# Kernel tuning notes

Measured on AMD Instinct MI355X. Metric: run time of the kernel, lower is better.

The kernel has to match this reference:

```python
import math
import jax, jax.numpy as jnp
import numpy as np

EPS = 1e-12

def _layernorm(x, g, b):
    u = x.mean(-1, keepdims=True)
    s = ((x - u) ** 2).mean(-1, keepdims=True)
    return g * (x - u) / jnp.sqrt(s + EPS) + b

def _sinusoidal_pe(S, d):
    pos = np.arange(S, dtype=np.float32)[:, None]
    div = np.exp(np.arange(0, d, 2, dtype=np.float32) * -(math.log(10000.0) / d))
    pe = np.zeros((S, d), dtype=np.float32)
    pe[:, 0::2] = np.sin(pos * div)
    pe[:, 1::2] = np.cos(pos * div)
    return jnp.asarray(pe)

def setup_inputs() -> dict:
    key = jax.random.key(0)
    k1, k2, k3, k4 = jax.random.split(key, 4)
    B, L, V, Dw, H = 32, 2048, 30522, 300, 768
    P = 16                      # separator period -> S = L // P ingredients per row
    S = L // P
    ids = jax.random.randint(k1, (B, L), 1, V).astype(jnp.int32)
    sep = np.zeros((B, L), dtype=np.int32)
    sep[:, P - 1::P] = 1        # a separator token every P tokens
    emb_table = jax.random.normal(k2, (V, Dw), dtype=jnp.float32) * 0.02
    emb_table = emb_table.at[0].set(0.0)  # padding_idx=0
    W = jax.random.normal(k3, (Dw, H), dtype=jnp.float32) * 0.02
    b = jnp.zeros((H,), dtype=jnp.float32)
    return {
        "ingr_input_ids": ids,
        "ingr_sep_masks": jnp.asarray(sep),
        "num_ingr": S,
        "emb_table": emb_table,
        "ln1_g": jnp.ones((Dw,), jnp.float32),
        "ln1_b": jnp.zeros((Dw,), jnp.float32),
        "W": W,
        "b": b,
        "ln2_g": jnp.ones((H,), jnp.float32),
        "ln2_b": jnp.zeros((H,), jnp.float32),
    }

def reference(ingr_input_ids, ingr_sep_masks, num_ingr,
              emb_table, ln1_g, ln1_b, W, b, ln2_g, ln2_b):
    S = int(num_ingr)
    H = W.shape[1]
    # embed + LN + Linear + ReLU + LN (dropout is identity at eval)
    e = emb_table[ingr_input_ids]                       # [B, L, Dw]
    h = _layernorm(e, ln1_g, ln1_b)
    h = jax.nn.relu(jnp.einsum('bld,dh->blh', h, W) + b)
    h = _layernorm(h, ln2_g, ln2_b)                     # [B, L, H]
    # ragged segment mean: segment id = exclusive cumsum of sep mask;
    # separator tokens (out[:-1] in the original) are excluded from the mean;
    # tokens after the last separator fall into bucket S and are dropped.
    sep = ingr_sep_masks
    seg = jnp.cumsum(sep, axis=1) - sep                 # [B, L]
    seg = jnp.minimum(seg, S)
    valid = (1 - sep).astype(h.dtype)                   # [B, L]
    seg_sum = jax.vmap(lambda hh, ss: jax.ops.segment_sum(hh, ss, num_segments=S + 1))(
        h * valid[..., None], seg)                      # [B, S+1, H]
    seg_cnt = jax.vmap(lambda vv, ss: jax.ops.segment_sum(vv, ss, num_segments=S + 1))(
        valid, seg)                                     # [B, S+1]
    mean = jnp.where(seg_cnt[..., None] > 0,
                     seg_sum / jnp.maximum(seg_cnt, 1.0)[..., None],
                     0.0)[:, :S]                        # [B, S, H]
    return mean + _sinusoidal_pe(S, H)[None]
```

## Files before the change

kernel.cpp:

```cpp
#include <hip/hip_runtime.h>
#include <hip/hip_bf16.h>

#define B_   32
#define L_   2048
#define V_   30522
#define DW   300
#define H_   768
#define KP   320
#define NT   (H_/16)
#define KT   (KP/32)
#define VPAD 30528
#define MB   48
#define NW   6
#define APAD 336

typedef __attribute__((ext_vector_type(8))) short bf16x8;
typedef __attribute__((ext_vector_type(4))) float f32x4;

__global__ void pack_w(const float* __restrict__ W, __hip_bfloat16* __restrict__ Wp) {
    int t = blockIdx.x * 256 + threadIdx.x;
    if (t >= NT * KT * 64) return;
    int lane = t & 63;
    int f    = t >> 6;
    int n    = f % NT;
    int kt   = f / NT;
    int col  = n * 16 + (lane & 15);
    int k0   = kt * 32 + (lane >> 4) * 8;
    union { __hip_bfloat16 h[8]; int4 v; } u;
    #pragma unroll
    for (int j = 0; j < 8; ++j) {
        int k = k0 + j;
        float w = (k < DW) ? W[(size_t)k * H_ + col] : 0.f;
        u.h[j] = __float2bfloat16(w);
    }
    reinterpret_cast<int4*>(Wp)[t] = u.v;
}

__global__ void embed_ln1(const float* __restrict__ emb, const float* __restrict__ g1,
                          const float* __restrict__ b1, __hip_bfloat16* __restrict__ h1) {
    int wave = (blockIdx.x * blockDim.x + threadIdx.x) >> 6;
    int lane = threadIdx.x & 63;
    if (wave >= VPAD) return;
    __hip_bfloat16* dst = h1 + (size_t)wave * KP;
    if (wave >= V_) {
        for (int k = lane; k < KP; k += 64) dst[k] = __float2bfloat16(0.f);
        return;
    }
    const float* row = emb + (size_t)wave * DW;
    float x[5]; float s = 0.f, ss = 0.f;
    #pragma unroll
    for (int i = 0; i < 5; ++i) {
        int k = lane + i * 64;
        float v = (k < DW) ? row[k] : 0.f;
        x[i] = v; s += v; ss += v * v;
    }
    #pragma unroll
    for (int m = 32; m >= 1; m >>= 1) { s += __shfl_xor(s, m); ss += __shfl_xor(ss, m); }
    float mu   = s / (float)DW;
    float var  = ss / (float)DW - mu * mu;
    float rstd = rsqrtf(var + 1e-12f);
    #pragma unroll
    for (int i = 0; i < 5; ++i) {
        int k = lane + i * 64;
        float o = (k < DW) ? (g1[k] * ((x[i] - mu) * rstd) + b1[k]) : 0.f;
        dst[k] = __float2bfloat16(o);
    }
}

__global__ void __launch_bounds__(512, 2)
gemm_ln2(const __hip_bfloat16* __restrict__ h1, const __hip_bfloat16* __restrict__ Wp,
         const float* __restrict__ bias, const float* __restrict__ g2,
         const float* __restrict__ b2, __hip_bfloat16* __restrict__ G) {
    __shared__ __hip_bfloat16 sA[MB * APAD];
    __shared__ float sred[2][8][MB];
    int tid  = threadIdx.x;
    int w    = tid >> 6;
    int lane = tid & 63;
    int r = lane & 15, q = lane >> 4;
    size_t row0 = (size_t)blockIdx.x * MB;

    const int4* gsrc = reinterpret_cast<const int4*>(h1 + row0 * KP);
    #pragma unroll
    for (int i = 0; i < 4; ++i) {
        int t4 = tid + i * 512;
        if (t4 < MB * KP / 8) {
            int row = t4 / 40;
            int col = (t4 % 40) * 8;
            *reinterpret_cast<int4*>(&sA[row * APAD + col]) = gsrc[t4];
        }
    }

    f32x4 acc[NW][3];
    #pragma unroll
    for (int nl = 0; nl < NW; ++nl)
        #pragma unroll
        for (int m = 0; m < 3; ++m) acc[nl][m] = (f32x4){0.f, 0.f, 0.f, 0.f};

    const bf16x8* Bv = reinterpret_cast<const bf16x8*>(Wp) + (size_t)w * NW * 64 + lane;
    const char* sAc = reinterpret_cast<const char*>(sA);
    const int abase = r * (APAD * 2) + q * 16;
    int phase = (int)(blockIdx.x % KT);

    bf16x8 bbuf[2][NW];
    bf16x8 abuf[2][3];

    {
        const bf16x8* bp = Bv + (size_t)phase * NT * 64;
        #pragma unroll
        for (int nl = 0; nl < NW; ++nl) bbuf[0][nl] = bp[nl * 64];
    }
    __syncthreads();
    #pragma unroll
    for (int m = 0; m < 3; ++m)
        abuf[0][m] = *reinterpret_cast<const bf16x8*>(
            sAc + abase + m * (16 * APAD * 2) + phase * 64);

    #pragma unroll
    for (int i = 0; i < KT; ++i) {
        const int cur = i & 1, nxt = (i + 1) & 1;
        if (i + 1 < KT) {
            int ktn = phase + i + 1; if (ktn >= KT) ktn -= KT;
            const bf16x8* bp = Bv + (size_t)ktn * NT * 64;
            #pragma unroll
            for (int nl = 0; nl < NW; ++nl) bbuf[nxt][nl] = bp[nl * 64];
            #pragma unroll
            for (int m = 0; m < 3; ++m)
                abuf[nxt][m] = *reinterpret_cast<const bf16x8*>(
                    sAc + abase + m * (16 * APAD * 2) + ktn * 64);
        }
        __builtin_amdgcn_sched_barrier(0);
        #pragma unroll
        for (int nl = 0; nl < NW; ++nl) {
            acc[nl][0] = __builtin_amdgcn_mfma_f32_16x16x32_bf16(abuf[cur][0], bbuf[cur][nl], acc[nl][0], 0, 0, 0);
            acc[nl][1] = __builtin_amdgcn_mfma_f32_16x16x32_bf16(abuf[cur][1], bbuf[cur][nl], acc[nl][1], 0, 0, 0);
            acc[nl][2] = __builtin_amdgcn_mfma_f32_16x16x32_bf16(abuf[cur][2], bbuf[cur][nl], acc[nl][2], 0, 0, 0);
        }
    }

    float s_[3][4], ss_[3][4];
    #pragma unroll
    for (int m = 0; m < 3; ++m)
        #pragma unroll
        for (int j = 0; j < 4; ++j) { s_[m][j] = 0.f; ss_[m][j] = 0.f; }
    #pragma unroll
    for (int nl = 0; nl < NW; ++nl) {
        float bn = bias[w * 96 + nl * 16 + r];
        #pragma unroll
        for (int m = 0; m < 3; ++m)
            #pragma unroll
            for (int j = 0; j < 4; ++j) {
                float v = acc[nl][m][j] + bn;
                v = v > 0.f ? v : 0.f;
                acc[nl][m][j] = v;
                s_[m][j] += v; ss_[m][j] += v * v;
            }
    }
    #pragma unroll
    for (int msk = 1; msk < 16; msk <<= 1)
        #pragma unroll
        for (int m = 0; m < 3; ++m)
            #pragma unroll
            for (int j = 0; j < 4; ++j) {
                s_[m][j]  += __shfl_xor(s_[m][j],  msk);
                ss_[m][j] += __shfl_xor(ss_[m][j], msk);
            }
    if (r == 0) {
        #pragma unroll
        for (int m = 0; m < 3; ++m)
            #pragma unroll
            for (int j = 0; j < 4; ++j) {
                int row = m * 16 + q * 4 + j;
                sred[0][w][row] = s_[m][j];
                sred[1][w][row] = ss_[m][j];
            }
    }
    __syncthreads();

    #pragma unroll
    for (int m = 0; m < 3; ++m) {
        #pragma unroll
        for (int j = 0; j < 4; ++j) {
            int row = m * 16 + q * 4 + j;
            float ts = 0.f, tss = 0.f;
            #pragma unroll
            for (int ww = 0; ww < 8; ++ww) { ts += sred[0][ww][row]; tss += sred[1][ww][row]; }
            float mu   = ts / (float)H_;
            float var  = tss / (float)H_ - mu * mu;
            float rstd = rsqrtf(var + 1e-12f);
            s_[m][j]  = mu;
            ss_[m][j] = rstd;
        }
    }
    #pragma unroll
    for (int nl = 0; nl < NW; ++nl) {
        int col = w * 96 + nl * 16 + r;
        float gg = g2[col], bb = b2[col];
        #pragma unroll
        for (int m = 0; m < 3; ++m)
            #pragma unroll
            for (int j = 0; j < 4; ++j) {
                size_t rowg = row0 + m * 16 + q * 4 + j;
                float val = gg * (acc[nl][m][j] - s_[m][j]) * ss_[m][j] + bb;
                G[rowg * H_ + col] = __float2bfloat16(val);
            }
    }
}

__global__ void sep_scan(const int* __restrict__ sep, int* __restrict__ pos, int* __restrict__ nsep) {
    int b = blockIdx.x;
    const int* row = sep + (size_t)b * L_;
    __shared__ int cnt[256];
    int tid = threadIdx.x;
    int local[8]; int c = 0;
    #pragma unroll
    for (int i = 0; i < 8; ++i) { int v = row[tid * 8 + i]; local[i] = v; c += v; }
    cnt[tid] = c; __syncthreads();
    for (int ofs = 1; ofs < 256; ofs <<= 1) {
        int v = (tid >= ofs) ? cnt[tid - ofs] : 0;
        __syncthreads();
        cnt[tid] += v;
        __syncthreads();
    }
    int w = cnt[tid] - c;
    #pragma unroll
    for (int i = 0; i < 8; ++i)
        if (local[i]) { pos[(size_t)b * L_ + w] = tid * 8 + i; ++w; }
    if (tid == 255) nsep[b] = cnt[255];
}

__global__ void seg_gather(const int* __restrict__ ids, const int* __restrict__ pos,
                           const int* __restrict__ nsep, const __hip_bfloat16* __restrict__ G,
                           float* __restrict__ out, int S) {
    int blk = blockIdx.x;
    int s = blk % S, b = blk / S;
    int tid = threadIdx.x;
    int ns = nsep[b];
    int lo, hi;
    if (s > ns) { lo = 1; hi = 0; }
    else {
        lo = (s == 0) ? 0 : pos[(size_t)b * L_ + (s - 1)] + 1;
        hi = (s < ns) ? pos[(size_t)b * L_ + s] - 1 : L_ - 1;
    }
    int cnt = hi - lo + 1; if (cnt < 0) cnt = 0;
    float a0 = 0.f, a1 = 0.f, a2 = 0.f;
    for (int t = lo; t <= hi; ++t) {
        int v = ids[(size_t)b * L_ + t];
        const __hip_bfloat16* gr = G + (size_t)v * H_;
        a0 += __bfloat162float(gr[tid]);
        a1 += __bfloat162float(gr[tid + 256]);
        a2 += __bfloat162float(gr[tid + 512]);
    }
    float inv = (cnt > 0) ? 1.f / (float)cnt : 0.f;
    float* orow = out + ((size_t)b * S + s) * H_;
    const float cexp = -9.210340371976184f / (float)H_;
    float acc[3] = {a0, a1, a2};
    #pragma unroll
    for (int c = 0; c < 3; ++c) {
        int n = tid + c * 256;
        int i = n >> 1;
        float div = expf((float)(2 * i) * cexp);
        float ang = (float)s * div;
        float pe  = (n & 1) ? cosf(ang) : sinf(ang);
        orow[n] = acc[c] * inv + pe;
    }
}

extern "C" void kernel_launch(void* const* d_in, const int* in_sizes, int n_in,
                              void* d_out, int out_size, void* d_ws, size_t ws_size,
                              hipStream_t stream) {
    const int*   ids  = (const int*)d_in[0];
    const int*   sep  = (const int*)d_in[1];
    const float* emb  = (const float*)d_in[3];
    const float* g1   = (const float*)d_in[4];
    const float* b1   = (const float*)d_in[5];
    const float* W    = (const float*)d_in[6];
    const float* bias = (const float*)d_in[7];
    const float* g2   = (const float*)d_in[8];
    const float* b2   = (const float*)d_in[9];
    float* out = (float*)d_out;

    int S = out_size / (B_ * H_);

    char* ws = (char*)d_ws;
    __hip_bfloat16* Wp  = (__hip_bfloat16*)(ws);
    __hip_bfloat16* h1  = (__hip_bfloat16*)(ws + 491520);
    __hip_bfloat16* G   = (__hip_bfloat16*)(ws + 491520 + 19537920);
    int* pos  = (int*)(ws + 491520 + 19537920 + 46891008);
    int* nsep = (int*)(ws + 491520 + 19537920 + 46891008 + 262144);
    (void)ws_size; (void)n_in; (void)in_sizes;

    pack_w   <<<(NT * KT * 64 + 255) / 256, 256, 0, stream>>>(W, Wp);
    embed_ln1<<<VPAD / 4, 256, 0, stream>>>(emb, g1, b1, h1);
    gemm_ln2 <<<VPAD / MB, 512, 0, stream>>>(h1, Wp, bias, g2, b2, G);
    sep_scan <<<B_, 256, 0, stream>>>(sep, pos, nsep);
    seg_gather<<<B_ * S, 256, 0, stream>>>(ids, pos, nsep, G, out, S);
}
```

Baseline: 82.92 us.

## Deepen GEMM B prefetch, vectorize segment gather, precompute PE table

The GEMM inner loop now keeps a 4-deep register ring for the W fragments, prefetching three K-steps ahead instead of one, so global-load latency is better hidden behind the MFMAs. seg_gather is restructured so 192 threads each read 16-byte vectors of the bf16 row, split the tokens between two groups and reduce through shared memory, replacing scalar 2-byte loads. Sinusoidal positional encodings are computed once by a new small kernel into workspace, so seg_gather no longer evaluates expf/sinf/cosf per element. The costs are extra register pressure in the GEMM, 64 idle threads per gather block, and one more kernel launch.

```diff
diff --git a/kernel.cpp b/kernel.cpp
--- a/kernel.cpp
+++ b/kernel.cpp
@@ -101,15 +101,17 @@
     const int abase = r * (APAD * 2) + q * 16;
     int phase = (int)(blockIdx.x % KT);
 
-    bf16x8 bbuf[2][NW];
+    bf16x8 bbuf[4][NW];
     bf16x8 abuf[2][3];
 
-    {
-        const bf16x8* bp = Bv + (size_t)phase * NT * 64;
-        #pragma unroll
-        for (int nl = 0; nl < NW; ++nl) bbuf[0][nl] = bp[nl * 64];
-    }
     __syncthreads();
+    #pragma unroll
+    for (int p = 0; p < 3; ++p) {
+        int ktp = phase + p; if (ktp >= KT) ktp -= KT;
+        const bf16x8* bp = Bv + (size_t)ktp * NT * 64;
+        #pragma unroll
+        for (int nl = 0; nl < NW; ++nl) bbuf[p][nl] = bp[nl * 64];
+    }
     #pragma unroll
     for (int m = 0; m < 3; ++m)
         abuf[0][m] = *reinterpret_cast<const bf16x8*>(
@@ -117,23 +119,26 @@
 
     #pragma unroll
     for (int i = 0; i < KT; ++i) {
-        const int cur = i & 1, nxt = (i + 1) & 1;
+        const int cur = i & 3, acur = i & 1;
+        if (i + 3 < KT) {
+            int ktn = phase + i + 3; if (ktn >= KT) ktn -= KT;
+            const bf16x8* bp = Bv + (size_t)ktn * NT * 64;
+            #pragma unroll
+            for (int nl = 0; nl < NW; ++nl) bbuf[(i + 3) & 3][nl] = bp[nl * 64];
+        }
         if (i + 1 < KT) {
             int ktn = phase + i + 1; if (ktn >= KT) ktn -= KT;
-            const bf16x8* bp = Bv + (size_t)ktn * NT * 64;
-            #pragma unroll
-            for (int nl = 0; nl < NW; ++nl) bbuf[nxt][nl] = bp[nl * 64];
             #pragma unroll
             for (int m = 0; m < 3; ++m)
-                abuf[nxt][m] = *reinterpret_cast<const bf16x8*>(
+                abuf[(i + 1) & 1][m] = *reinterpret_cast<const bf16x8*>(
                     sAc + abase + m * (16 * APAD * 2) + ktn * 64);
         }
         __builtin_amdgcn_sched_barrier(0);
         #pragma unroll
         for (int nl = 0; nl < NW; ++nl) {
-            acc[nl][0] = __builtin_amdgcn_mfma_f32_16x16x32_bf16(abuf[cur][0], bbuf[cur][nl], acc[nl][0], 0, 0, 0);
-            acc[nl][1] = __builtin_amdgcn_mfma_f32_16x16x32_bf16(abuf[cur][1], bbuf[cur][nl], acc[nl][1], 0, 0, 0);
-            acc[nl][2] = __builtin_amdgcn_mfma_f32_16x16x32_bf16(abuf[cur][2], bbuf[cur][nl], acc[nl][2], 0, 0, 0);
+            acc[nl][0] = __builtin_amdgcn_mfma_f32_16x16x32_bf16(abuf[acur][0], bbuf[cur][nl], acc[nl][0], 0, 0, 0);
+            acc[nl][1] = __builtin_amdgcn_mfma_f32_16x16x32_bf16(abuf[acur][1], bbuf[cur][nl], acc[nl][1], 0, 0, 0);
+            acc[nl][2] = __builtin_amdgcn_mfma_f32_16x16x32_bf16(abuf[acur][2], bbuf[cur][nl], acc[nl][2], 0, 0, 0);
         }
     }
 
@@ -228,12 +233,23 @@
     if (tid == 255) nsep[b] = cnt[255];
 }
 
+__global__ void pe_table(float* __restrict__ PE, int S) {
+    int t = blockIdx.x * 256 + threadIdx.x;
+    if (t >= S * H_) return;
+    int s = t / H_, n = t % H_;
+    const float cexp = -9.210340371976184f / (float)H_;
+    float div = expf((float)(2 * (n >> 1)) * cexp);
+    float ang = (float)s * div;
+    PE[t] = (n & 1) ? cosf(ang) : sinf(ang);
+}
+
 __global__ void seg_gather(const int* __restrict__ ids, const int* __restrict__ pos,
                            const int* __restrict__ nsep, const __hip_bfloat16* __restrict__ G,
-                           float* __restrict__ out, int S) {
+                           const float* __restrict__ PE, float* __restrict__ out, int S) {
     int blk = blockIdx.x;
     int s = blk % S, b = blk / S;
     int tid = threadIdx.x;
+    int g = tid / 96, l = tid - g * 96;
     int ns = nsep[b];
     int lo, hi;
     if (s > ns) { lo = 1; hi = 0; }
@@ -242,26 +258,35 @@
         hi = (s < ns) ? pos[(size_t)b * L_ + s] - 1 : L_ - 1;
     }
     int cnt = hi - lo + 1; if (cnt < 0) cnt = 0;
-    float a0 = 0.f, a1 = 0.f, a2 = 0.f;
-    for (int t = lo; t <= hi; ++t) {
-        int v = ids[(size_t)b * L_ + t];
-        const __hip_bfloat16* gr = G + (size_t)v * H_;
-        a0 += __bfloat162float(gr[tid]);
-        a1 += __bfloat162float(gr[tid + 256]);
-        a2 += __bfloat162float(gr[tid + 512]);
-    }
-    float inv = (cnt > 0) ? 1.f / (float)cnt : 0.f;
-    float* orow = out + ((size_t)b * S + s) * H_;
-    const float cexp = -9.210340371976184f / (float)H_;
-    float acc[3] = {a0, a1, a2};
-    #pragma unroll
-    for (int c = 0; c < 3; ++c) {
-        int n = tid + c * 256;
-        int i = n >> 1;
-        float div = expf((float)(2 * i) * cexp);
-        float ang = (float)s * div;
-        float pe  = (n & 1) ? cosf(ang) : sinf(ang);
-        orow[n] = acc[c] * inv + pe;
+
+    float a[8] = {0.f, 0.f, 0.f, 0.f, 0.f, 0.f, 0.f, 0.f};
+    if (g < 2) {
+        for (int t = lo + g; t <= hi; t += 2) {
+            int v = ids[(size_t)b * L_ + t];
+            int4 raw = *reinterpret_cast<const int4*>(G + (size_t)v * H_ + l * 8);
+            const unsigned short* u = reinterpret_cast<const unsigned short*>(&raw);
+            #pragma unroll
+            for (int k = 0; k < 8; ++k) {
+                union { unsigned int i; float f; } c; c.i = ((unsigned int)u[k]) << 16;
+                a[k] += c.f;
+            }
+        }
+    }
+    __shared__ float red[96 * 8];
+    if (g == 1) {
+        #pragma unroll
+        for (int k = 0; k < 8; ++k) red[l * 8 + k] = a[k];
+    }
+    __syncthreads();
+    if (g == 0) {
+        float inv = (cnt > 0) ? 1.f / (float)cnt : 0.f;
+        float* orow = out + ((size_t)b * S + s) * H_;
+        const float* pe = PE + (size_t)s * H_;
+        #pragma unroll
+        for (int k = 0; k < 8; ++k) {
+            int n = l * 8 + k;
+            orow[n] = (a[k] + red[l * 8 + k]) * inv + pe[n];
+        }
     }
 }
 
@@ -285,13 +310,15 @@
     __hip_bfloat16* Wp  = (__hip_bfloat16*)(ws);
     __hip_bfloat16* h1  = (__hip_bfloat16*)(ws + 491520);
     __hip_bfloat16* G   = (__hip_bfloat16*)(ws + 491520 + 19537920);
-    int* pos  = (int*)(ws + 491520 + 19537920 + 46891008);
-    int* nsep = (int*)(ws + 491520 + 19537920 + 46891008 + 262144);
+    int*   pos  = (int*)(ws + 491520 + 19537920 + 46891008);
+    int*   nsep = (int*)(ws + 491520 + 19537920 + 46891008 + 262144);
+    float* PE   = (float*)(ws + 491520 + 19537920 + 46891008 + 262144 + 256);
     (void)ws_size; (void)n_in; (void)in_sizes;
 
     pack_w   <<<(NT * KT * 64 + 255) / 256, 256, 0, stream>>>(W, Wp);
+    pe_table <<<(S * H_ + 255) / 256, 256, 0, stream>>>(PE, S);
     embed_ln1<<<VPAD / 4, 256, 0, stream>>>(emb, g1, b1, h1);
     gemm_ln2 <<<VPAD / MB, 512, 0, stream>>>(h1, Wp, bias, g2, b2, G);
     sep_scan <<<B_, 256, 0, stream>>>(sep, pos, nsep);
-    seg_gather<<<B_ * S, 256, 0, stream>>>(ids, pos, nsep, G, out, S);
-}
+    seg_gather<<<B_ * S, 256, 0, stream>>>(ids, pos, nsep, G, PE, out, S);
+}
```

After: 86.62 us. 4.5% more time.
